# Kernel tuning notes

Measured on AMD Instinct MI355X. Metric: run time of the kernel, lower is better.

## Reference

```python
import jax, jax.numpy as jnp
import numpy as np

N, E, IN_DIM, HID, HEADS, OUT_DIM, T = 50000, 200000, 32, 64, 4, 32, 3
NEG_SLOPE = 0.2  # PyG GATv2Conv default


def setup_inputs() -> dict:
    key = jax.random.key(0)
    ks = jax.random.split(key, 16)
    s = 0.1
    return {
        "feat": jax.random.normal(ks[0], (N, IN_DIM), jnp.float32),
        "W_in": jax.random.normal(ks[1], (IN_DIM, HID), jnp.float32) * s,
        "b_in": jnp.zeros((HID,), jnp.float32),
        "Wl": jax.random.normal(ks[2], (2 * HID, HEADS * HID), jnp.float32) * s,
        "bl": jnp.zeros((HEADS * HID,), jnp.float32),
        "Wr": jax.random.normal(ks[3], (2 * HID, HEADS * HID), jnp.float32) * s,
        "br": jnp.zeros((HEADS * HID,), jnp.float32),
        "att": jax.random.normal(ks[4], (HEADS, HID), jnp.float32) * s,
        "b_conv": jnp.zeros((HEADS * HID,), jnp.float32),
        "Wg": jax.random.normal(ks[5], (HID, OUT_DIM), jnp.float32) * s,
        "bg": jnp.zeros((OUT_DIM,), jnp.float32),
        "edge_index": jax.random.randint(ks[6], (2, E), 0, N, jnp.int32),
        "node_mask": jax.random.randint(ks[7], (N,), 0, T + 1, jnp.int32),
        "current_state": jax.random.randint(ks[8], (N,), 0, 2, jnp.int32),
    }


def reference(feat, W_in, b_in, Wl, bl, Wr, br, att, b_conv, Wg, bg,
              edge_index, node_mask, current_state):
    # add self loops (GATv2Conv add_self_loops=True)
    loops = jnp.arange(N, dtype=edge_index.dtype)
    src = jnp.concatenate([edge_index[0], loops])  # [E+N]
    dst = jnp.concatenate([edge_index[1], loops])

    h0 = feat @ W_in + b_in  # [N, HID]
    bias_sum = b_conv.reshape(HEADS, HID).sum(0)  # heads are summed after bias add

    def step(h, i):
        active = node_mask > i  # [N] bool: nodes updated at this step
        x = jnp.concatenate([h, h0], axis=-1)  # [N, 2*HID]
        xl = (x @ Wl + bl).reshape(N, HEADS, HID)  # source transform
        xr = (x @ Wr + br).reshape(N, HEADS, HID)  # target transform
        e_act = active[src] & active[dst]  # edge alive iff both endpoints active
        s = jax.nn.leaky_relu(xl[src] + xr[dst], NEG_SLOPE)  # [E+N, H, C]
        score = jnp.einsum('ehc,hc->eh', s, att)  # [E+N, H]
        score = jnp.where(e_act[:, None], score, -1e30)
        smax = jax.lax.stop_gradient(
            jax.ops.segment_max(score, dst, num_segments=N))  # [N, H]
        ex = jnp.exp(score - smax[dst]) * e_act[:, None].astype(score.dtype)
        denom = jax.ops.segment_sum(ex, dst, num_segments=N)  # [N, H]
        alpha = ex / jnp.maximum(denom[dst], 1e-16)  # segment softmax per dst
        msg = alpha[:, :, None] * xl[src]  # [E+N, H, C]
        agg = jax.ops.segment_sum(msg, dst, num_segments=N)  # [N, H, C]
        out = jnp.tanh(agg.sum(1) + bias_sum)  # sum over heads, then Tanh
        return jnp.where(active[:, None], out, h), None

    h, _ = jax.lax.scan(step, h0, jnp.arange(T))
    # original returns g_embed(h[current_state]); fixed-shape variant: mask rows
    out = (h @ Wg + bg) * (current_state[:, None] > 0).astype(h.dtype)
    return out
```

## Files before the change

### kernel.cpp

```cpp
#include <hip/hip_runtime.h>
#include <hip/hip_bf16.h>

#define NN      50000
#define EE      200000
#define IN_DIM  32
#define HID     64
#define HEADS   4
#define OUTD    32
#define TSTEPS  3

typedef unsigned short bf16_t;
typedef __attribute__((ext_vector_type(8))) short  short8;
typedef __attribute__((ext_vector_type(4))) float  floatx4;

__device__ __forceinline__ float b2f(bf16_t u) {
    union { unsigned int i; float f; } v; v.i = ((unsigned int)u) << 16; return v.f;
}
__device__ __forceinline__ bf16_t f2b(float f) {
    union { float f; unsigned int i; } v; v.f = f;
    unsigned int r = v.i + 0x7FFF + ((v.i >> 16) & 1);
    return (bf16_t)(r >> 16);
}

#define H0_BLOCKS ((NN + 31) / 32)

__global__ __launch_bounds__(256) void k_setup(
        const void* W_in, const void* b_in, const void* att, const void* bconv,
        const void* Wg, const void* bg,
        const void* Wl_raw, const void* Wr_raw, const void* bl_raw, const void* br_raw,
        const void* feat_raw,
        float* attf, float* bcf, float* Wgf, float* bgf,
        bf16_t* __restrict__ Wt, bf16_t* __restrict__ WtS, float* __restrict__ bb,
        int* __restrict__ deg, int* __restrict__ flag, int* __restrict__ mbuf,
        bf16_t* __restrict__ h0, bf16_t* __restrict__ h) {
    __shared__ int bad;
    __shared__ float Ws[IN_DIM * HID];
    __shared__ float bs[HID];
    int t = threadIdx.x, bid = blockIdx.x;
    if (t == 0) bad = 0;
    __syncthreads();
    {
        const bf16_t* p = (const bf16_t*)W_in;
        int mybad = 0;
        for (int i = t; i < IN_DIM * HID; i += 256) {
            float v = b2f(p[i]);
            if (v != v || fabsf(v) > 100.f) mybad = 1;
        }
        if (mybad) atomicOr(&bad, 1);
    }
    __syncthreads();
    int f = bad ? 0 : 1;
    if (bid == 0 && t == 0) *flag = f;

    if (bid < 256) {
        int i = bid * 256 + t;
        int n = i >> 7, k = i & 127;
        const void* W = (n < 256) ? Wl_raw : Wr_raw;
        int nn = (n < 256) ? n : n - 256;
        float v = f ? b2f(((const bf16_t*)W)[k * 256 + nn])
                    : ((const float*)W)[k * 256 + nn];
        Wt[n * 128 + k] = f2b(v);
        if (k < 64) {
            float v2 = f ? b2f(((const bf16_t*)W)[(k + 64) * 256 + nn])
                         : ((const float*)W)[(k + 64) * 256 + nn];
            WtS[n * 64 + k] = f2b(v + v2);
        }
        if (k == 0) {
            const void* b = (n < 256) ? bl_raw : br_raw;
            bb[n] = f ? b2f(((const bf16_t*)b)[nn]) : ((const float*)b)[nn];
        }
    } else if (bid < 267) {
        int i = (bid - 256) * 256 + t;
        const void* src; float* dst; int off;
        if      (i < 256)  { src = att;   dst = attf; off = i; }
        else if (i < 512)  { src = bconv; dst = bcf;  off = i - 256; }
        else if (i < 2560) { src = Wg;    dst = Wgf;  off = i - 512; }
        else if (i < 2592) { src = bg;    dst = bgf;  off = i - 2560; }
        else return;
        dst[off] = f ? b2f(((const bf16_t*)src)[off]) : ((const float*)src)[off];
    } else if (bid < 463) {
        int i = (bid - 267) * 256 + t;
        if (i < NN) deg[i] = 0;
        if (bid == 267 && t < 16) mbuf[t] = 0;
    } else {
        for (int i = t; i < IN_DIM * HID; i += 256)
            Ws[i] = f ? b2f(((const bf16_t*)W_in)[i]) : ((const float*)W_in)[i];
        if (t < HID)
            bs[t] = f ? b2f(((const bf16_t*)b_in)[t]) : ((const float*)b_in)[t];
        __syncthreads();
        int nb = bid - 463;
        int wid = t >> 6, c = t & 63;
#pragma unroll
        for (int g = 0; g < 8; g++) {
            int node = (nb * 8 + g) * 4 + wid;
            if (node >= NN) break;
            float acc = bs[c];
            if (f) {
                const bf16_t* fr = (const bf16_t*)feat_raw + (size_t)node * IN_DIM;
#pragma unroll
                for (int k = 0; k < IN_DIM; k++) acc += b2f(fr[k]) * Ws[k * HID + c];
            } else {
                const float* fr = (const float*)feat_raw + (size_t)node * IN_DIM;
#pragma unroll
                for (int k = 0; k < IN_DIM; k++) acc += fr[k] * Ws[k * HID + c];
            }
            bf16_t o = f2b(acc);
            h0[(size_t)node * HID + c] = o;
            h [(size_t)node * HID + c] = o;
        }
    }
}

__global__ __launch_bounds__(256) void k_hist_all(const int* __restrict__ dst,
                                                  const int* __restrict__ mask,
                                                  int* __restrict__ deg,
                                                  int* __restrict__ mbuf) {
    int t = threadIdx.x, bid = blockIdx.x;
    int i = bid * 256 + t;
    if (i < EE) atomicAdd(&deg[dst[i]], 1);
    if (bid < (NN + 255) / 256) {
        __shared__ int wcnt[4][4];
        int wid = t >> 6, lane = t & 63;
        int ni = bid * 256 + t;
        bool valid = ni < NN;
        int v = 0;
        if (valid) { int m = mask[ni]; v = m < 0 ? 0 : (m > 3 ? 3 : m); }
#pragma unroll
        for (int b = 0; b < 4; b++) {
            unsigned long long mm = __ballot(valid && v == b);
            if (lane == 0) wcnt[wid][b] = __popcll(mm);
        }
        __syncthreads();
        if (t < 4) {
            int s = wcnt[0][t] + wcnt[1][t] + wcnt[2][t] + wcnt[3][t];
            if (s) atomicAdd(&mbuf[t], s);
        }
    }
}

__global__ __launch_bounds__(256) void k_scan_partial(const int* __restrict__ deg,
                                                      int* __restrict__ part, int n) {
    __shared__ int sd[256];
    int t = threadIdx.x;
    int base = blockIdx.x * 1024;
    int s = 0;
#pragma unroll
    for (int j = 0; j < 4; j++) {
        int i = base + t * 4 + j;
        if (i < n) s += deg[i];
    }
    sd[t] = s; __syncthreads();
    for (int off = 128; off > 0; off >>= 1) {
        if (t < off) sd[t] += sd[t + off];
        __syncthreads();
    }
    if (t == 0) part[blockIdx.x] = sd[0];
}

__global__ __launch_bounds__(256) void k_scan_final(const int* __restrict__ deg,
                                                    const int* __restrict__ part,
                                                    int* __restrict__ row_ptr,
                                                    int* __restrict__ cursor,
                                                    int n, int nch,
                                                    int* __restrict__ mbuf) {
    __shared__ int sc[256];
    __shared__ int bpref;
    int t = threadIdx.x;
    int bid = blockIdx.x;
    if (t == 0) {
        int acc = 0;
        for (int i = 0; i < bid; i++) acc += part[i];
        bpref = acc;
        if (bid == 0) {
            int tot = 0;
            for (int i = 0; i < nch; i++) tot += part[i];
            row_ptr[n] = tot;
            int c1 = mbuf[1], c2 = mbuf[2], c3 = mbuf[3];
            mbuf[7] = 0;
            mbuf[6] = c3;
            mbuf[5] = c3 + c2;
            mbuf[4] = c3 + c2 + c1;
            mbuf[8] = c3 + c2 + c1;
            mbuf[9] = c3 + c2;
            mbuf[10] = c3;
        }
    }
    int base = bid * 1024;
    int v[4]; int s = 0;
#pragma unroll
    for (int j = 0; j < 4; j++) {
        int i = base + t * 4 + j;
        v[j] = (i < n) ? deg[i] : 0;
        s += v[j];
    }
    sc[t] = s; __syncthreads();
    for (int off = 1; off < 256; off <<= 1) {
        int add = (t >= off) ? sc[t - off] : 0;
        __syncthreads();
        sc[t] += add;
        __syncthreads();
    }
    int run = sc[t] - s + bpref;
#pragma unroll
    for (int j = 0; j < 4; j++) {
        int i = base + t * 4 + j;
        if (i < n) { row_ptr[i] = run; cursor[i] = run; run += v[j]; }
    }
}

__global__ __launch_bounds__(256) void k_scatter_all(const int* __restrict__ src,
                                                     const int* __restrict__ dst,
                                                     int* __restrict__ cursor,
                                                     int* __restrict__ col,
                                                     const int* __restrict__ mask,
                                                     int* __restrict__ mbuf,
                                                     int* __restrict__ order) {
    int t = threadIdx.x, bid = blockIdx.x;
    int i = bid * 256 + t;
    if (i < EE) {
        int sv = src[i];
        int m = mask[sv]; m = m < 0 ? 0 : (m > 3 ? 3 : m);
        int d = dst[i];
        int pos = atomicAdd(&cursor[d], 1);
        col[pos] = sv | (m << 28);
    }
    if (bid < (NN + 255) / 256) {
        __shared__ int wcnt[4][4];
        __shared__ int bbase[4];
        int wid = t >> 6, lane = t & 63;
        int ni = bid * 256 + t;
        bool valid = ni < NN;
        int v = 0;
        if (valid) { int m = mask[ni]; v = m < 0 ? 0 : (m > 3 ? 3 : m); }
        int rank = 0;
#pragma unroll
        for (int b = 0; b < 4; b++) {
            unsigned long long mm = __ballot(valid && v == b);
            if (valid && v == b)
                rank = __popcll(mm & ((lane == 0) ? 0ull : (~0ull >> (64 - lane))));
            if (lane == 0) wcnt[wid][b] = __popcll(mm);
        }
        __syncthreads();
        if (t < 4) {
            int tot = wcnt[0][t] + wcnt[1][t] + wcnt[2][t] + wcnt[3][t];
            bbase[t] = atomicAdd(&mbuf[4 + t], tot);
        }
        __syncthreads();
        if (valid) {
            int wpre = 0;
            for (int ww = 0; ww < wid; ww++) wpre += wcnt[ww][v];
            order[bbase[v] + wpre + rank] = ni;
        }
    }
}

__global__ __launch_bounds__(256) void k_gemm0(const bf16_t* __restrict__ h0,
                                               const bf16_t* __restrict__ WtS,
                                               const float* __restrict__ bb,
                                               bf16_t* __restrict__ xl,
                                               bf16_t* __restrict__ xr,
                                               const int* __restrict__ order,
                                               const int* __restrict__ mbuf) {
    int count = mbuf[8];
    int mbase = blockIdx.x * 64;
    if (mbase >= count) return;

    __shared__ bf16_t smem[64 * 72 + 128 * 72];
    bf16_t* As = smem;
    bf16_t* Bs = smem + 64 * 72;
    bf16_t* Cs = smem;

    int t = threadIdx.x;
    int nbase = blockIdx.y * 128;

    {
        int ln = t >> 2, lq = t & 3;
        int idx = mbase + ln;
        int node = (idx < count) ? order[idx] : -1;
        ulonglong2 z; z.x = 0; z.y = 0;
        ulonglong2 v0 = z, v1 = z;
        if (node >= 0) {
            v0 = *(const ulonglong2*)(h0 + (size_t)node * HID + lq * 16);
            v1 = *(const ulonglong2*)(h0 + (size_t)node * HID + lq * 16 + 8);
        }
        *(ulonglong2*)(&As[ln * 72 + lq * 16]) = v0;
        *(ulonglong2*)(&As[ln * 72 + lq * 16 + 8]) = v1;
    }
    {
        int n = t >> 1, kc = (t & 1) * 32;
        const bf16_t* srcp = WtS + (size_t)(nbase + n) * 64 + kc;
        bf16_t* dstp = &Bs[n * 72 + kc];
        *(ulonglong2*)(dstp)      = *(const ulonglong2*)(srcp);
        *(ulonglong2*)(dstp + 8)  = *(const ulonglong2*)(srcp + 8);
        *(ulonglong2*)(dstp + 16) = *(const ulonglong2*)(srcp + 16);
        *(ulonglong2*)(dstp + 24) = *(const ulonglong2*)(srcp + 24);
    }
    __syncthreads();

    int wv = t >> 6, lane = t & 63, mrow = lane & 15, quad = lane >> 4;
    floatx4 acc[8];
#pragma unroll
    for (int nf = 0; nf < 8; nf++) acc[nf] = (floatx4){0.f, 0.f, 0.f, 0.f};
#pragma unroll
    for (int kq = 0; kq < 2; kq++) {
        short8 a = *(const short8*)(&As[(wv * 16 + mrow) * 72 + kq * 32 + quad * 8]);
#pragma unroll
        for (int nf = 0; nf < 8; nf++) {
            short8 b = *(const short8*)(&Bs[(nf * 16 + mrow) * 72 + kq * 32 + quad * 8]);
            acc[nf] = __builtin_amdgcn_mfma_f32_16x16x32_bf16(a, b, acc[nf], 0, 0, 0);
        }
    }
    __syncthreads();

#pragma unroll
    for (int nf = 0; nf < 8; nf++) {
        float bv = bb[nbase + nf * 16 + mrow];
#pragma unroll
        for (int r = 0; r < 4; r++) {
            int m = wv * 16 + quad * 4 + r;
            Cs[m * 136 + nf * 16 + mrow] = f2b(acc[nf][r] + bv);
        }
    }
    __syncthreads();

    bf16_t* outp = (blockIdx.y < 2) ? xl : xr;
    int cc = (blockIdx.y & 1) * 128;
#pragma unroll
    for (int i = 0; i < 4; i++) {
        int c = t + i * 256;
        int m = c >> 4, kc = (c & 15) * 8;
        int idx = mbase + m;
        if (idx < count) {
            int node = order[idx];
            *(ulonglong2*)(outp + (size_t)node * 256 + cc + kc) =
                *(const ulonglong2*)(&Cs[m * 136 + kc]);
        }
    }
}

__global__ __launch_bounds__(256) void k_gemm_mfma(const bf16_t* __restrict__ h,
                                                   const bf16_t* __restrict__ h0,
                                                   const bf16_t* __restrict__ Wt,
                                                   const float* __restrict__ bb,
                                                   bf16_t* __restrict__ xl,
                                                   bf16_t* __restrict__ xr,
                                                   const int* __restrict__ order,
                                                   const int* __restrict__ mbuf,
                                                   int step) {
    int count = mbuf[8 + step];
    int mbase = blockIdx.x * 64;
    if (mbase >= count) return;

    __shared__ bf16_t smem[64 * 136 + 128 * 136];
    bf16_t* As = smem;
    bf16_t* Bs = smem + 64 * 136;
    bf16_t* Cs = smem;

    int t = threadIdx.x;
    int nbase = blockIdx.y * 128;

    {
        int ln = t >> 2, lq = t & 3;
        int idx = mbase + ln;
        int node = (idx < count) ? order[idx] : -1;
        ulonglong2 z; z.x = 0; z.y = 0;
#pragma unroll
        for (int j = 0; j < 2; j++) {
            int chunk = lq + j * 4;
            ulonglong2 vh = z, vh0 = z;
            if (node >= 0) {
                vh  = *(const ulonglong2*)(h  + (size_t)node * HID + chunk * 8);
                vh0 = *(const ulonglong2*)(h0 + (size_t)node * HID + chunk * 8);
            }
            *(ulonglong2*)(&As[ln * 136 + chunk * 8]) = vh;
            *(ulonglong2*)(&As[ln * 136 + 64 + chunk * 8]) = vh0;
        }
    }
#pragma unroll
    for (int i = 0; i < 8; i++) {
        int c = t + i * 256;
        int n = c >> 4, kc = (c & 15) * 8;
        *(ulonglong2*)(&Bs[n * 136 + kc]) =
            *(const ulonglong2*)(Wt + (size_t)(nbase + n) * 128 + kc);
    }
    __syncthreads();

    int wv = t >> 6, lane = t & 63, mrow = lane & 15, quad = lane >> 4;
    floatx4 acc[8];
#pragma unroll
    for (int nf = 0; nf < 8; nf++) acc[nf] = (floatx4){0.f, 0.f, 0.f, 0.f};
#pragma unroll
    for (int kq = 0; kq < 4; kq++) {
        short8 a = *(const short8*)(&As[(wv * 16 + mrow) * 136 + kq * 32 + quad * 8]);
#pragma unroll
        for (int nf = 0; nf < 8; nf++) {
            short8 b = *(const short8*)(&Bs[(nf * 16 + mrow) * 136 + kq * 32 + quad * 8]);
            acc[nf] = __builtin_amdgcn_mfma_f32_16x16x32_bf16(a, b, acc[nf], 0, 0, 0);
        }
    }
    __syncthreads();

#pragma unroll
    for (int nf = 0; nf < 8; nf++) {
        float bv = bb[nbase + nf * 16 + mrow];
#pragma unroll
        for (int r = 0; r < 4; r++) {
            int m = wv * 16 + quad * 4 + r;
            Cs[m * 136 + nf * 16 + mrow] = f2b(acc[nf][r] + bv);
        }
    }
    __syncthreads();

    bf16_t* outp = (blockIdx.y < 2) ? xl : xr;
    int cc = (blockIdx.y & 1) * 128;
#pragma unroll
    for (int i = 0; i < 4; i++) {
        int c = t + i * 256;
        int m = c >> 4, kc = (c & 15) * 8;
        int idx = mbase + m;
        if (idx < count) {
            int node = order[idx];
            *(ulonglong2*)(outp + (size_t)node * 256 + cc + kc) =
                *(const ulonglong2*)(&Cs[m * 136 + kc]);
        }
    }
}

__global__ __launch_bounds__(256) void k_agg(bf16_t* __restrict__ h,
                                             const bf16_t* __restrict__ xl,
                                             const bf16_t* __restrict__ xr,
                                             const float* __restrict__ att,
                                             const float* __restrict__ b_conv,
                                             const int* __restrict__ row_ptr,
                                             const int* __restrict__ col,
                                             const int* __restrict__ order,
                                             const int* __restrict__ mbuf,
                                             int step) {
    int count = mbuf[8 + step];
    int wid = threadIdx.x >> 6;
    int lane = threadIdx.x & 63;
    float4 attv = *(const float4*)(att + lane * 4);
    float4 bcv  = *(const float4*)(b_conv + lane * 4);

    for (int idx = blockIdx.x * 4 + wid; idx < count; idx += gridDim.x * 4) {
        int node = order[idx];

        ushort4 xru = *(const ushort4*)(xr + (size_t)node * 256 + lane * 4);
        float xr0 = b2f(xru.x), xr1 = b2f(xru.y), xr2 = b2f(xru.z), xr3 = b2f(xru.w);

        float a0 = 0.f, a1 = 0.f, a2 = 0.f, a3 = 0.f, l = 0.f;

        auto do_edge = [&](int s) {
            ushort4 xu = *(const ushort4*)(xl + (size_t)s * 256 + lane * 4);
            float x0 = b2f(xu.x), x1 = b2f(xu.y), x2 = b2f(xu.z), x3 = b2f(xu.w);
            float v0 = x0 + xr0; v0 = v0 > 0.f ? v0 : 0.2f * v0;
            float v1 = x1 + xr1; v1 = v1 > 0.f ? v1 : 0.2f * v1;
            float v2 = x2 + xr2; v2 = v2 > 0.f ? v2 : 0.2f * v2;
            float v3 = x3 + xr3; v3 = v3 > 0.f ? v3 : 0.2f * v3;
            float part = attv.x * v0 + attv.y * v1 + attv.z * v2 + attv.w * v3;
            part += __shfl_xor(part, 1, 64);
            part += __shfl_xor(part, 2, 64);
            part += __shfl_xor(part, 4, 64);
            part += __shfl_xor(part, 8, 64);
            float p = __expf(part);
            l += p;
            a0 += p * x0; a1 += p * x1; a2 += p * x2; a3 += p * x3;
        };

        do_edge(node);
        int e0 = row_ptr[node], e1 = row_ptr[node + 1];
        int e = e0;
        for (; e + 3 < e1; e += 4) {
            int c0 = col[e], c1 = col[e + 1], c2 = col[e + 2], c3 = col[e + 3];
            if (((unsigned)c0 >> 28) > (unsigned)step) do_edge(c0 & 0x0FFFFFFF);
            if (((unsigned)c1 >> 28) > (unsigned)step) do_edge(c1 & 0x0FFFFFFF);
            if (((unsigned)c2 >> 28) > (unsigned)step) do_edge(c2 & 0x0FFFFFFF);
            if (((unsigned)c3 >> 28) > (unsigned)step) do_edge(c3 & 0x0FFFFFFF);
        }
        for (; e < e1; e++) {
            int c = col[e];
            if (((unsigned)c >> 28) > (unsigned)step) do_edge(c & 0x0FFFFFFF);
        }

        float inv = 1.f / l;
        float t0 = a0 * inv + bcv.x;
        float t1 = a1 * inv + bcv.y;
        float t2 = a2 * inv + bcv.z;
        float t3 = a3 * inv + bcv.w;
        t0 += __shfl_xor(t0, 16, 64); t0 += __shfl_xor(t0, 32, 64);
        t1 += __shfl_xor(t1, 16, 64); t1 += __shfl_xor(t1, 32, 64);
        t2 += __shfl_xor(t2, 16, 64); t2 += __shfl_xor(t2, 32, 64);
        t3 += __shfl_xor(t3, 16, 64); t3 += __shfl_xor(t3, 32, 64);
        if (lane < 16) {
            ushort4 o;
            o.x = f2b(tanhf(t0)); o.y = f2b(tanhf(t1));
            o.z = f2b(tanhf(t2)); o.w = f2b(tanhf(t3));
            *(ushort4*)(h + (size_t)node * HID + lane * 4) = o;
        }
    }
}

__global__ __launch_bounds__(256) void k_out(const bf16_t* __restrict__ h,
                                             const float* __restrict__ Wg,
                                             const float* __restrict__ bg,
                                             const int* __restrict__ cs,
                                             void* __restrict__ out,
                                             const int* __restrict__ flag) {
    __shared__ float Ws[HID * OUTD];
    __shared__ float bs[OUTD];
    int t = threadIdx.x;
    for (int i = t; i < HID * OUTD; i += 256) Ws[i] = Wg[i];
    if (t < OUTD) bs[t] = bg[t];
    __syncthreads();
    int node = blockIdx.x * 8 + (t >> 5);
    int c = t & 31;
    if (node >= NN) return;
    float res = 0.f;
    if (cs[node] > 0) {
        const bf16_t* hr = h + (size_t)node * HID;
        float acc = bs[c];
#pragma unroll
        for (int k = 0; k < HID; k++) acc += b2f(hr[k]) * Ws[k * OUTD + c];
        res = acc;
    }
    size_t idx = (size_t)node * OUTD + c;
    if (*flag) ((bf16_t*)out)[idx] = f2b(res);
    else       ((float*)out)[idx]  = res;
}

static inline size_t alignup(size_t x) { return (x + 255) & ~(size_t)255; }

extern "C" void kernel_launch(void* const* d_in, const int* in_sizes, int n_in,
                              void* d_out, int out_size, void* d_ws, size_t ws_size,
                              hipStream_t stream) {
    const void* feat_raw  = d_in[0];
    const void* W_in_raw  = d_in[1];
    const void* b_in_raw  = d_in[2];
    const void* Wl_raw    = d_in[3];
    const void* bl_raw    = d_in[4];
    const void* Wr_raw    = d_in[5];
    const void* br_raw    = d_in[6];
    const void* att_raw   = d_in[7];
    const void* bconv_raw = d_in[8];
    const void* Wg_raw    = d_in[9];
    const void* bg_raw    = d_in[10];
    const int* edge       = (const int*)d_in[11];
    const int* nmask      = (const int*)d_in[12];
    const int* cstate     = (const int*)d_in[13];

    const int* e_src = edge;
    const int* e_dst = edge + EE;

    const size_t SZ_HB   = alignup((size_t)NN * HID * sizeof(bf16_t));
    const size_t SZ_X    = alignup((size_t)NN * 256 * sizeof(bf16_t));
    const size_t SZ_I    = alignup((size_t)NN * sizeof(int));
    const size_t SZ_RP   = alignup((size_t)(NN + 1) * sizeof(int));
    const size_t SZ_COL  = alignup((size_t)EE * sizeof(int));
    const int nch = (NN + 1023) / 1024;
    const size_t SZ_PART = alignup((size_t)(nch + 1) * sizeof(int));
    const size_t SZ_WT   = alignup((size_t)512 * 128 * sizeof(bf16_t));
    const size_t SZ_WTS  = alignup((size_t)512 * 64 * sizeof(bf16_t));
    const size_t SZ_B    = alignup(512 * sizeof(float));
    const size_t SZ_WG   = alignup((size_t)HID * OUTD * sizeof(float));

    char* w = (char*)d_ws;
    bf16_t* h0   = (bf16_t*)w; w += SZ_HB;
    bf16_t* h    = (bf16_t*)w; w += SZ_HB;
    bf16_t* xl   = (bf16_t*)w; w += SZ_X;
    bf16_t* xr   = (bf16_t*)w; w += SZ_X;
    int* deg     = (int*)w;    w += SZ_I;
    int* row_ptr = (int*)w;    w += SZ_RP;
    int* cursor  = (int*)w;    w += SZ_I;
    int* colA    = (int*)w;    w += SZ_COL;
    int* order   = (int*)w;    w += SZ_I;
    int* part    = (int*)w;    w += SZ_PART;
    bf16_t* Wt   = (bf16_t*)w; w += SZ_WT;
    bf16_t* WtS  = (bf16_t*)w; w += SZ_WTS;
    float* bb    = (float*)w;  w += SZ_B;
    float* attf  = (float*)w;  w += SZ_B;
    float* bcf   = (float*)w;  w += SZ_B;
    float* Wgf   = (float*)w;  w += SZ_WG;
    float* bgf   = (float*)w;  w += SZ_B;
    int* flag    = (int*)w;    w += 256;
    int* mbuf    = (int*)w;    w += 256;
    if ((size_t)(w - (char*)d_ws) > ws_size) return;

    k_setup<<<463 + H0_BLOCKS, 256, 0, stream>>>(
        W_in_raw, b_in_raw, att_raw, bconv_raw, Wg_raw, bg_raw,
        Wl_raw, Wr_raw, bl_raw, br_raw, feat_raw,
        attf, bcf, Wgf, bgf, Wt, WtS, bb, deg, flag, mbuf, h0, h);

    k_hist_all<<<(EE + 255) / 256, 256, 0, stream>>>(e_dst, nmask, deg, mbuf);
    k_scan_partial<<<nch, 256, 0, stream>>>(deg, part, NN);
    k_scan_final<<<nch, 256, 0, stream>>>(deg, part, row_ptr, cursor, NN, nch, mbuf);
    k_scatter_all<<<(EE + 255) / 256, 256, 0, stream>>>(e_src, e_dst, cursor, colA,
                                                        nmask, mbuf, order);

    k_gemm0<<<dim3((NN + 63) / 64, 4), 256, 0, stream>>>(h0, WtS, bb, xl, xr, order, mbuf);
    k_agg<<<2048, 256, 0, stream>>>(h, xl, xr, attf, bcf, row_ptr, colA, order, mbuf, 0);

    for (int s = 1; s < TSTEPS; s++) {
        k_gemm_mfma<<<dim3((NN + 63) / 64, 4), 256, 0, stream>>>(h, h0, Wt, bb, xl, xr,
                                                                 order, mbuf, s);
        k_agg<<<2048, 256, 0, stream>>>(h, xl, xr, attf, bcf,
                                        row_ptr, colA, order, mbuf, s);
    }

    k_out<<<(NN + 7) / 8, 256, 0, stream>>>(h, Wgf, bgf, cstate, d_out, flag);
}
```

Measured before the change: 251.0 us.

## Fuse GEMM, aggregation and output stages into one cooperative persistent kernel

Replaces the seven per-step launches (gemm0, agg, gemm, agg, gemm, agg, out) with a single cooperative kernel. The kernel loops over tiles with a grid-stride schedule and separates stages with grid-wide barriers. This removes launch overhead and inter-kernel gaps. In exchange the grid is limited to occupancy-bounded residency with the largest shared-memory footprint, and each stage now pays a grid.sync, which may cut parallelism for the aggregation stage.

```diff
diff --git a/kernel.cpp b/kernel.cpp
--- a/kernel.cpp
+++ b/kernel.cpp
@@ -1,5 +1,8 @@
 #include <hip/hip_runtime.h>
 #include <hip/hip_bf16.h>
+#include <hip/hip_cooperative_groups.h>
+
+namespace cg = cooperative_groups;
 
 #define NN      50000
 #define EE      200000
@@ -254,189 +257,182 @@
     }
 }
 
-__global__ __launch_bounds__(256) void k_gemm0(const bf16_t* __restrict__ h0,
-                                               const bf16_t* __restrict__ WtS,
-                                               const float* __restrict__ bb,
-                                               bf16_t* __restrict__ xl,
-                                               bf16_t* __restrict__ xr,
-                                               const int* __restrict__ order,
-                                               const int* __restrict__ mbuf) {
-    int count = mbuf[8];
-    int mbase = blockIdx.x * 64;
-    if (mbase >= count) return;
-
-    __shared__ bf16_t smem[64 * 72 + 128 * 72];
+
+__device__ void dev_gemm64(const bf16_t* __restrict__ h0,
+                           const bf16_t* __restrict__ WtS,
+                           const float* __restrict__ bb,
+                           bf16_t* __restrict__ xl, bf16_t* __restrict__ xr,
+                           const int* __restrict__ order, int count,
+                           bf16_t* smem) {
     bf16_t* As = smem;
     bf16_t* Bs = smem + 64 * 72;
     bf16_t* Cs = smem;
-
     int t = threadIdx.x;
-    int nbase = blockIdx.y * 128;
-
-    {
-        int ln = t >> 2, lq = t & 3;
-        int idx = mbase + ln;
-        int node = (idx < count) ? order[idx] : -1;
-        ulonglong2 z; z.x = 0; z.y = 0;
-        ulonglong2 v0 = z, v1 = z;
-        if (node >= 0) {
-            v0 = *(const ulonglong2*)(h0 + (size_t)node * HID + lq * 16);
-            v1 = *(const ulonglong2*)(h0 + (size_t)node * HID + lq * 16 + 8);
-        }
-        *(ulonglong2*)(&As[ln * 72 + lq * 16]) = v0;
-        *(ulonglong2*)(&As[ln * 72 + lq * 16 + 8]) = v1;
-    }
-    {
-        int n = t >> 1, kc = (t & 1) * 32;
-        const bf16_t* srcp = WtS + (size_t)(nbase + n) * 64 + kc;
-        bf16_t* dstp = &Bs[n * 72 + kc];
-        *(ulonglong2*)(dstp)      = *(const ulonglong2*)(srcp);
-        *(ulonglong2*)(dstp + 8)  = *(const ulonglong2*)(srcp + 8);
-        *(ulonglong2*)(dstp + 16) = *(const ulonglong2*)(srcp + 16);
-        *(ulonglong2*)(dstp + 24) = *(const ulonglong2*)(srcp + 24);
-    }
-    __syncthreads();
-
-    int wv = t >> 6, lane = t & 63, mrow = lane & 15, quad = lane >> 4;
-    floatx4 acc[8];
-#pragma unroll
-    for (int nf = 0; nf < 8; nf++) acc[nf] = (floatx4){0.f, 0.f, 0.f, 0.f};
-#pragma unroll
-    for (int kq = 0; kq < 2; kq++) {
-        short8 a = *(const short8*)(&As[(wv * 16 + mrow) * 72 + kq * 32 + quad * 8]);
+    int ntiles = ((count + 63) >> 6) * 4;
+    for (int tile = blockIdx.x; tile < ntiles; tile += gridDim.x) {
+        int mbase = (tile >> 2) * 64;
+        int yt = tile & 3;
+        int nbase = yt * 128;
+        {
+            int ln = t >> 2, lq = t & 3;
+            int idx = mbase + ln;
+            int node = (idx < count) ? order[idx] : -1;
+            ulonglong2 z; z.x = 0; z.y = 0;
+            ulonglong2 v0 = z, v1 = z;
+            if (node >= 0) {
+                v0 = *(const ulonglong2*)(h0 + (size_t)node * HID + lq * 16);
+                v1 = *(const ulonglong2*)(h0 + (size_t)node * HID + lq * 16 + 8);
+            }
+            *(ulonglong2*)(&As[ln * 72 + lq * 16]) = v0;
+            *(ulonglong2*)(&As[ln * 72 + lq * 16 + 8]) = v1;
+        }
+        {
+            int n = t >> 1, kc = (t & 1) * 32;
+            const bf16_t* srcp = WtS + (size_t)(nbase + n) * 64 + kc;
+            bf16_t* dstp = &Bs[n * 72 + kc];
+            *(ulonglong2*)(dstp)      = *(const ulonglong2*)(srcp);
+            *(ulonglong2*)(dstp + 8)  = *(const ulonglong2*)(srcp + 8);
+            *(ulonglong2*)(dstp + 16) = *(const ulonglong2*)(srcp + 16);
+            *(ulonglong2*)(dstp + 24) = *(const ulonglong2*)(srcp + 24);
+        }
+        __syncthreads();
+
+        int wv = t >> 6, lane = t & 63, mrow = lane & 15, quad = lane >> 4;
+        floatx4 acc[8];
+#pragma unroll
+        for (int nf = 0; nf < 8; nf++) acc[nf] = (floatx4){0.f, 0.f, 0.f, 0.f};
+#pragma unroll
+        for (int kq = 0; kq < 2; kq++) {
+            short8 a = *(const short8*)(&As[(wv * 16 + mrow) * 72 + kq * 32 + quad * 8]);
+#pragma unroll
+            for (int nf = 0; nf < 8; nf++) {
+                short8 b = *(const short8*)(&Bs[(nf * 16 + mrow) * 72 + kq * 32 + quad * 8]);
+                acc[nf] = __builtin_amdgcn_mfma_f32_16x16x32_bf16(a, b, acc[nf], 0, 0, 0);
+            }
+        }
+        __syncthreads();
+
 #pragma unroll
         for (int nf = 0; nf < 8; nf++) {
-            short8 b = *(const short8*)(&Bs[(nf * 16 + mrow) * 72 + kq * 32 + quad * 8]);
-            acc[nf] = __builtin_amdgcn_mfma_f32_16x16x32_bf16(a, b, acc[nf], 0, 0, 0);
-        }
-    }
-    __syncthreads();
-
-#pragma unroll
-    for (int nf = 0; nf < 8; nf++) {
-        float bv = bb[nbase + nf * 16 + mrow];
-#pragma unroll
-        for (int r = 0; r < 4; r++) {
-            int m = wv * 16 + quad * 4 + r;
-            Cs[m * 136 + nf * 16 + mrow] = f2b(acc[nf][r] + bv);
-        }
-    }
-    __syncthreads();
-
-    bf16_t* outp = (blockIdx.y < 2) ? xl : xr;
-    int cc = (blockIdx.y & 1) * 128;
-#pragma unroll
-    for (int i = 0; i < 4; i++) {
-        int c = t + i * 256;
-        int m = c >> 4, kc = (c & 15) * 8;
-        int idx = mbase + m;
-        if (idx < count) {
-            int node = order[idx];
-            *(ulonglong2*)(outp + (size_t)node * 256 + cc + kc) =
-                *(const ulonglong2*)(&Cs[m * 136 + kc]);
-        }
-    }
-}
-
-__global__ __launch_bounds__(256) void k_gemm_mfma(const bf16_t* __restrict__ h,
-                                                   const bf16_t* __restrict__ h0,
-                                                   const bf16_t* __restrict__ Wt,
-                                                   const float* __restrict__ bb,
-                                                   bf16_t* __restrict__ xl,
-                                                   bf16_t* __restrict__ xr,
-                                                   const int* __restrict__ order,
-                                                   const int* __restrict__ mbuf,
-                                                   int step) {
-    int count = mbuf[8 + step];
-    int mbase = blockIdx.x * 64;
-    if (mbase >= count) return;
-
-    __shared__ bf16_t smem[64 * 136 + 128 * 136];
+            float bv = bb[nbase + nf * 16 + mrow];
+#pragma unroll
+            for (int r = 0; r < 4; r++) {
+                int m = wv * 16 + quad * 4 + r;
+                Cs[m * 136 + nf * 16 + mrow] = f2b(acc[nf][r] + bv);
+            }
+        }
+        __syncthreads();
+
+        bf16_t* outp = (yt < 2) ? xl : xr;
+        int cc = (yt & 1) * 128;
+#pragma unroll
+        for (int i = 0; i < 4; i++) {
+            int c = t + i * 256;
+            int m = c >> 4, kc = (c & 15) * 8;
+            int idx = mbase + m;
+            if (idx < count) {
+                int node = order[idx];
+                *(ulonglong2*)(outp + (size_t)node * 256 + cc + kc) =
+                    *(const ulonglong2*)(&Cs[m * 136 + kc]);
+            }
+        }
+        __syncthreads();
+    }
+}
+
+__device__ void dev_gemm128(const bf16_t* __restrict__ h,
+                            const bf16_t* __restrict__ h0,
+                            const bf16_t* __restrict__ Wt,
+                            const float* __restrict__ bb,
+                            bf16_t* __restrict__ xl, bf16_t* __restrict__ xr,
+                            const int* __restrict__ order, int count,
+                            bf16_t* smem) {
     bf16_t* As = smem;
     bf16_t* Bs = smem + 64 * 136;
     bf16_t* Cs = smem;
-
     int t = threadIdx.x;
-    int nbase = blockIdx.y * 128;
-
-    {
-        int ln = t >> 2, lq = t & 3;
-        int idx = mbase + ln;
-        int node = (idx < count) ? order[idx] : -1;
-        ulonglong2 z; z.x = 0; z.y = 0;
-#pragma unroll
-        for (int j = 0; j < 2; j++) {
-            int chunk = lq + j * 4;
-            ulonglong2 vh = z, vh0 = z;
-            if (node >= 0) {
-                vh  = *(const ulonglong2*)(h  + (size_t)node * HID + chunk * 8);
-                vh0 = *(const ulonglong2*)(h0 + (size_t)node * HID + chunk * 8);
-            }
-            *(ulonglong2*)(&As[ln * 136 + chunk * 8]) = vh;
-            *(ulonglong2*)(&As[ln * 136 + 64 + chunk * 8]) = vh0;
-        }
-    }
-#pragma unroll
-    for (int i = 0; i < 8; i++) {
-        int c = t + i * 256;
-        int n = c >> 4, kc = (c & 15) * 8;
-        *(ulonglong2*)(&Bs[n * 136 + kc]) =
-            *(const ulonglong2*)(Wt + (size_t)(nbase + n) * 128 + kc);
-    }
-    __syncthreads();
-
-    int wv = t >> 6, lane = t & 63, mrow = lane & 15, quad = lane >> 4;
-    floatx4 acc[8];
-#pragma unroll
-    for (int nf = 0; nf < 8; nf++) acc[nf] = (floatx4){0.f, 0.f, 0.f, 0.f};
-#pragma unroll
-    for (int kq = 0; kq < 4; kq++) {
-        short8 a = *(const short8*)(&As[(wv * 16 + mrow) * 136 + kq * 32 + quad * 8]);
+    int ntiles = ((count + 63) >> 6) * 4;
+    for (int tile = blockIdx.x; tile < ntiles; tile += gridDim.x) {
+        int mbase = (tile >> 2) * 64;
+        int yt = tile & 3;
+        int nbase = yt * 128;
+        {
+            int ln = t >> 2, lq = t & 3;
+            int idx = mbase + ln;
+            int node = (idx < count) ? order[idx] : -1;
+            ulonglong2 z; z.x = 0; z.y = 0;
+#pragma unroll
+            for (int j = 0; j < 2; j++) {
+                int chunk = lq + j * 4;
+                ulonglong2 vh = z, vh0 = z;
+                if (node >= 0) {
+                    vh  = *(const ulonglong2*)(h  + (size_t)node * HID + chunk * 8);
+                    vh0 = *(const ulonglong2*)(h0 + (size_t)node * HID + chunk * 8);
+                }
+                *(ulonglong2*)(&As[ln * 136 + chunk * 8]) = vh;
+                *(ulonglong2*)(&As[ln * 136 + 64 + chunk * 8]) = vh0;
+            }
+        }
+#pragma unroll
+        for (int i = 0; i < 8; i++) {
+            int c = t + i * 256;
+            int n = c >> 4, kc = (c & 15) * 8;
+            *(ulonglong2*)(&Bs[n * 136 + kc]) =
+                *(const ulonglong2*)(Wt + (size_t)(nbase + n) * 128 + kc);
+        }
+        __syncthreads();
+
+        int wv = t >> 6, lane = t & 63, mrow = lane & 15, quad = lane >> 4;
+        floatx4 acc[8];
+#pragma unroll
+        for (int nf = 0; nf < 8; nf++) acc[nf] = (floatx4){0.f, 0.f, 0.f, 0.f};
+#pragma unroll
+        for (int kq = 0; kq < 4; kq++) {
+            short8 a = *(const short8*)(&As[(wv * 16 + mrow) * 136 + kq * 32 + quad * 8]);
+#pragma unroll
+            for (int nf = 0; nf < 8; nf++) {
+                short8 b = *(const short8*)(&Bs[(nf * 16 + mrow) * 136 + kq * 32 + quad * 8]);
+                acc[nf] = __builtin_amdgcn_mfma_f32_16x16x32_bf16(a, b, acc[nf], 0, 0, 0);
+            }
+        }
+        __syncthreads();
+
 #pragma unroll
         for (int nf = 0; nf < 8; nf++) {
-            short8 b = *(const short8*)(&Bs[(nf * 16 + mrow) * 136 + kq * 32 + quad * 8]);
-            acc[nf] = __builtin_amdgcn_mfma_f32_16x16x32_bf16(a, b, acc[nf], 0, 0, 0);
-        }
-    }
-    __syncthreads();
-
-#pragma unroll
-    for (int nf = 0; nf < 8; nf++) {
-        float bv = bb[nbase + nf * 16 + mrow];
-#pragma unroll
-        for (int r = 0; r < 4; r++) {
-            int m = wv * 16 + quad * 4 + r;
-            Cs[m * 136 + nf * 16 + mrow] = f2b(acc[nf][r] + bv);
-        }
-    }
-    __syncthreads();
-
-    bf16_t* outp = (blockIdx.y < 2) ? xl : xr;
-    int cc = (blockIdx.y & 1) * 128;
-#pragma unroll
-    for (int i = 0; i < 4; i++) {
-        int c = t + i * 256;
-        int m = c >> 4, kc = (c & 15) * 8;
-        int idx = mbase + m;
-        if (idx < count) {
-            int node = order[idx];
-            *(ulonglong2*)(outp + (size_t)node * 256 + cc + kc) =
-                *(const ulonglong2*)(&Cs[m * 136 + kc]);
-        }
-    }
-}
-
-__global__ __launch_bounds__(256) void k_agg(bf16_t* __restrict__ h,
-                                             const bf16_t* __restrict__ xl,
-                                             const bf16_t* __restrict__ xr,
-                                             const float* __restrict__ att,
-                                             const float* __restrict__ b_conv,
-                                             const int* __restrict__ row_ptr,
-                                             const int* __restrict__ col,
-                                             const int* __restrict__ order,
-                                             const int* __restrict__ mbuf,
-                                             int step) {
-    int count = mbuf[8 + step];
+            float bv = bb[nbase + nf * 16 + mrow];
+#pragma unroll
+            for (int r = 0; r < 4; r++) {
+                int m = wv * 16 + quad * 4 + r;
+                Cs[m * 136 + nf * 16 + mrow] = f2b(acc[nf][r] + bv);
+            }
+        }
+        __syncthreads();
+
+        bf16_t* outp = (yt < 2) ? xl : xr;
+        int cc = (yt & 1) * 128;
+#pragma unroll
+        for (int i = 0; i < 4; i++) {
+            int c = t + i * 256;
+            int m = c >> 4, kc = (c & 15) * 8;
+            int idx = mbase + m;
+            if (idx < count) {
+                int node = order[idx];
+                *(ulonglong2*)(outp + (size_t)node * 256 + cc + kc) =
+                    *(const ulonglong2*)(&Cs[m * 136 + kc]);
+            }
+        }
+        __syncthreads();
+    }
+}
+
+__device__ void dev_agg(bf16_t* __restrict__ h,
+                        const bf16_t* __restrict__ xl,
+                        const bf16_t* __restrict__ xr,
+                        const float* __restrict__ att,
+                        const float* __restrict__ b_conv,
+                        const int* __restrict__ row_ptr,
+                        const int* __restrict__ col,
+                        const int* __restrict__ order, int count, int step) {
     int wid = threadIdx.x >> 6;
     int lane = threadIdx.x & 63;
     float4 attv = *(const float4*)(att + lane * 4);
@@ -500,32 +496,59 @@
     }
 }
 
-__global__ __launch_bounds__(256) void k_out(const bf16_t* __restrict__ h,
-                                             const float* __restrict__ Wg,
-                                             const float* __restrict__ bg,
-                                             const int* __restrict__ cs,
-                                             void* __restrict__ out,
-                                             const int* __restrict__ flag) {
-    __shared__ float Ws[HID * OUTD];
-    __shared__ float bs[OUTD];
+__device__ void dev_out(const bf16_t* __restrict__ h,
+                        const float* __restrict__ Wg,
+                        const float* __restrict__ bg,
+                        const int* __restrict__ cs,
+                        void* __restrict__ out, int flagv, bf16_t* smem) {
+    float* Ws = (float*)smem;
+    float* bs = (float*)smem + 2048;
     int t = threadIdx.x;
     for (int i = t; i < HID * OUTD; i += 256) Ws[i] = Wg[i];
     if (t < OUTD) bs[t] = bg[t];
     __syncthreads();
-    int node = blockIdx.x * 8 + (t >> 5);
-    int c = t & 31;
-    if (node >= NN) return;
-    float res = 0.f;
-    if (cs[node] > 0) {
-        const bf16_t* hr = h + (size_t)node * HID;
-        float acc = bs[c];
-#pragma unroll
-        for (int k = 0; k < HID; k++) acc += b2f(hr[k]) * Ws[k * OUTD + c];
-        res = acc;
-    }
-    size_t idx = (size_t)node * OUTD + c;
-    if (*flag) ((bf16_t*)out)[idx] = f2b(res);
-    else       ((float*)out)[idx]  = res;
+    int nb_tot = (NN + 7) / 8;
+    for (int nb = blockIdx.x; nb < nb_tot; nb += gridDim.x) {
+        int node = nb * 8 + (t >> 5);
+        int c = t & 31;
+        if (node < NN) {
+            float res = 0.f;
+            if (cs[node] > 0) {
+                const bf16_t* hr = h + (size_t)node * HID;
+                float acc = bs[c];
+#pragma unroll
+                for (int k = 0; k < HID; k++) acc += b2f(hr[k]) * Ws[k * OUTD + c];
+                res = acc;
+            }
+            size_t idx = (size_t)node * OUTD + c;
+            if (flagv) ((bf16_t*)out)[idx] = f2b(res);
+            else       ((float*)out)[idx]  = res;
+        }
+    }
+}
+
+__global__ __launch_bounds__(256) void k_mega(
+        bf16_t* h, const bf16_t* h0, const bf16_t* Wt, const bf16_t* WtS,
+        const float* bb, const float* attf, const float* bcf,
+        const int* row_ptr, const int* colA, const int* order, const int* mbuf,
+        const float* Wgf, const float* bgf, const int* cstate, void* out,
+        const int* flag, bf16_t* xl, bf16_t* xr) {
+    __shared__ bf16_t smem[64 * 136 + 128 * 136];
+    cg::grid_group grid = cg::this_grid();
+
+    dev_gemm64(h0, WtS, bb, xl, xr, order, mbuf[8], smem);
+    grid.sync();
+    dev_agg(h, xl, xr, attf, bcf, row_ptr, colA, order, mbuf[8], 0);
+    grid.sync();
+    dev_gemm128(h, h0, Wt, bb, xl, xr, order, mbuf[9], smem);
+    grid.sync();
+    dev_agg(h, xl, xr, attf, bcf, row_ptr, colA, order, mbuf[9], 1);
+    grid.sync();
+    dev_gemm128(h, h0, Wt, bb, xl, xr, order, mbuf[10], smem);
+    grid.sync();
+    dev_agg(h, xl, xr, attf, bcf, row_ptr, colA, order, mbuf[10], 2);
+    grid.sync();
+    dev_out(h, Wgf, bgf, cstate, out, *flag, smem);
 }
 
 static inline size_t alignup(size_t x) { return (x + 255) & ~(size_t)255; }
@@ -596,15 +619,24 @@
     k_scatter_all<<<(EE + 255) / 256, 256, 0, stream>>>(e_src, e_dst, cursor, colA,
                                                         nmask, mbuf, order);
 
-    k_gemm0<<<dim3((NN + 63) / 64, 4), 256, 0, stream>>>(h0, WtS, bb, xl, xr, order, mbuf);
-    k_agg<<<2048, 256, 0, stream>>>(h, xl, xr, attf, bcf, row_ptr, colA, order, mbuf, 0);
-
-    for (int s = 1; s < TSTEPS; s++) {
-        k_gemm_mfma<<<dim3((NN + 63) / 64, 4), 256, 0, stream>>>(h, h0, Wt, bb, xl, xr,
-                                                                 order, mbuf, s);
-        k_agg<<<2048, 256, 0, stream>>>(h, xl, xr, attf, bcf,
-                                        row_ptr, colA, order, mbuf, s);
-    }
-
-    k_out<<<(NN + 7) / 8, 256, 0, stream>>>(h, Wgf, bgf, cstate, d_out, flag);
-}
+    int occ = 0;
+    if (hipOccupancyMaxActiveBlocksPerMultiprocessor(&occ, k_mega, 256, 0) != hipSuccess
+        || occ < 1) occ = 2;
+    int ncu = 256;
+    {
+        int dev = 0;
+        if (hipGetDevice(&dev) == hipSuccess) {
+            int v = 0;
+            if (hipDeviceGetAttribute(&v, hipDeviceAttributeMultiprocessorCount, dev)
+                == hipSuccess && v > 0) ncu = v;
+        }
+    }
+    dim3 grid(occ * ncu), block(256);
+    void* out_p = d_out;
+    void* kargs[] = {
+        (void*)&h, (void*)&h0, (void*)&Wt, (void*)&WtS, (void*)&bb,
+        (void*)&attf, (void*)&bcf, (void*)&row_ptr, (void*)&colA, (void*)&order,
+        (void*)&mbuf, (void*)&Wgf, (void*)&bgf, (void*)&cstate, (void*)&out_p,
+        (void*)&flag, (void*)&xl, (void*)&xr };
+    hipLaunchCooperativeKernel((const void*)k_mega, grid, block, kargs, 0, stream);
+}
```

Measured after the change: 648.3 us. 158% more time.
